# Kernel tuning notes

Measured on AMD Instinct MI355X. Metric: run time of the kernel, lower is better.

Reference implementation:

```python
import jax, jax.numpy as jnp
import numpy as np

N, E, IN_DIM, HID, OUT = 50000, 600000, 128, 256, 128

def setup_inputs() -> dict:
    key = jax.random.key(0)
    k1, k2, k3, k4, k5, k6, k7 = jax.random.split(key, 7)
    h = jax.random.normal(k1, (N, IN_DIM), dtype=jnp.float32)
    src = jax.random.randint(k2, (E,), 0, N)
    dst = jax.random.randint(k3, (E,), 0, N)
    s1 = 1.0 / np.sqrt(2 * IN_DIM)
    s2 = 1.0 / np.sqrt(HID)
    W1 = jax.random.uniform(k4, (2 * IN_DIM, HID), minval=-s1, maxval=s1, dtype=jnp.float32)
    b1 = jax.random.uniform(k5, (HID,), minval=-s1, maxval=s1, dtype=jnp.float32)
    W2 = jax.random.uniform(k6, (HID, OUT), minval=-s2, maxval=s2, dtype=jnp.float32)
    b2 = jax.random.uniform(k7, (OUT,), minval=-s2, maxval=s2, dtype=jnp.float32)
    return {"h": h, "src": src, "dst": dst, "W1": W1, "b1": b1, "W2": W2, "b2": b2}

def reference(h, src, dst, W1, b1, W2, b2):
    n = h.shape[0]
    # copy_u + mean: gather src features, segment-sum at dst, divide by in-degree
    msg_sum = jax.ops.segment_sum(h[src], dst, num_segments=n)          # [N, D]
    deg = jax.ops.segment_sum(jnp.ones((src.shape[0],), h.dtype), dst, num_segments=n)
    h_neigh = msg_sum / jnp.maximum(deg, 1.0)[:, None]                  # zero-deg nodes -> 0
    h_total = jnp.concatenate([h, h_neigh], axis=1)                     # [N, 2D]
    out = (h_total @ W1 + b1) @ W2 + b2                                 # 2-layer MLP (no inner activation)
    return jax.nn.relu(out)
```

## Files before the change

kernel.cpp:

```cpp
#include <hip/hip_runtime.h>

#define N_NODES 50000
#define E_EDGES 600000
#define IN_DIM  128
#define HID     256
#define OUT_DIM 128
#define CAP     64
#define ZROW    N_NODES

#define RANGE_N 6250
#define CHUNK_E 2048
#define NB_FILL 2344
#define NB_HCVT 3125
#define NB_WCVT 384
#define NB_PREP (NB_FILL + NB_HCVT + NB_WCVT + 1)
#define NB_MLP  782

typedef __bf16 bf16x8 __attribute__((ext_vector_type(8)));
typedef float  f32x16 __attribute__((ext_vector_type(16)));
typedef unsigned short ushort8 __attribute__((ext_vector_type(8)));

__device__ __forceinline__ unsigned short f2bf(float f) {
    union { float f; unsigned int i; } v; v.f = f;
    unsigned int b = v.i;
    b += 0x7fffu + ((b >> 16) & 1u);
    return (unsigned short)(b >> 16);
}
__device__ __forceinline__ void acc2(unsigned u, float& a0, float& a1) {
    union { unsigned i; float f; } lo, hi;
    lo.i = u << 16; hi.i = u & 0xffff0000u;
    a0 += lo.f; a1 += hi.f;
}

__global__ void __launch_bounds__(256)
sage_prep(const int* __restrict__ src, const int* __restrict__ dst,
          int* __restrict__ counts, char* __restrict__ outb,
          const float* __restrict__ h, unsigned short* __restrict__ ht,
          const float* __restrict__ W1, const float* __restrict__ W2,
          unsigned short* __restrict__ w1sw, unsigned short* __restrict__ w2sw) {
    int b = blockIdx.x;
    if (b < NB_FILL) {
        int r = b & 7;
        int chunk = b >> 3;
        int e0 = chunk * CHUNK_E + threadIdx.x * 8;
        if (e0 < E_EDGES) {
            int lo = r * RANGE_N, hi = lo + RANGE_N;
            const int4 d0 = *(const int4*)(dst + e0);
            const int4 d1 = *(const int4*)(dst + e0 + 4);
            int dd[8] = {d0.x, d0.y, d0.z, d0.w, d1.x, d1.y, d1.z, d1.w};
            #pragma unroll
            for (int k = 0; k < 8; ++k) {
                int d = dd[k];
                if (d >= lo && d < hi) {
                    int s = src[e0 + k];
                    int sl = atomicAdd(counts + d, 1);
                    if (sl < CAP) *((int*)(outb + (size_t)d * 512 + 256) + sl) = s;
                }
            }
        }
    } else if (b < NB_FILL + NB_HCVT) {
        int idx = (b - NB_FILL) * 256 + threadIdx.x;
        int n = idx >> 4, g = idx & 15;
        const float4 v0 = *(const float4*)(h + (size_t)n * IN_DIM + g * 8);
        const float4 v1 = *(const float4*)(h + (size_t)n * IN_DIM + g * 8 + 4);
        ushort8 o;
        o[0] = f2bf(v0.x); o[1] = f2bf(v0.y); o[2] = f2bf(v0.z); o[3] = f2bf(v0.w);
        o[4] = f2bf(v1.x); o[5] = f2bf(v1.y); o[6] = f2bf(v1.z); o[7] = f2bf(v1.w);
        *(ushort8*)(ht + (size_t)n * 128 + g * 8) = o;
    } else if (b < NB_FILL + NB_HCVT + NB_WCVT) {
        int i1 = (b - NB_FILL - NB_HCVT) * 256 + threadIdx.x;
        if (i1 < 65536) {
            int j = i1 & 7, n = (i1 >> 3) & 255, g = (i1 >> 11) & 1, ks = (i1 >> 12) & 3, c = i1 >> 14;
            int k = c * 64 + ks * 16 + g * 8 + j;
            w1sw[i1] = f2bf(W1[(size_t)k * HID + n]);
        } else {
            int i2 = i1 - 65536;
            int j = i2 & 7, n = (i2 >> 3) & 127, g = (i2 >> 10) & 1, ks = (i2 >> 11) & 7, c = (i2 >> 14) & 1;
            int k = c * 128 + ks * 16 + g * 8 + j;
            w2sw[i2] = f2bf(W2[(size_t)k * OUT_DIM + n]);
        }
    } else {
        if (threadIdx.x < 64)
            *(unsigned*)(ht + (size_t)ZROW * 128 + threadIdx.x * 2) = 0u;
    }
}

__global__ void __launch_bounds__(256, 4)
sage_fused(const int* __restrict__ counts,
           const unsigned short* __restrict__ ht,
           const unsigned short* __restrict__ w1sw,
           const unsigned short* __restrict__ w2sw,
           const float* __restrict__ b1,
           const float* __restrict__ b2,
           float* out) {
    __shared__ unsigned short hid_s[64][264];

    const int t = threadIdx.x;
    const int nw = t >> 6;
    const int lane = t & 63;
    const int lr = lane & 31;
    const int lg = lane >> 5;
    const int base = blockIdx.x * 64;

    {
        #pragma unroll 1
        for (int g = 0; g < 4; ++g) {
            const int m0 = nw * 16 + g * 4;
            float a0[4], a1[4];
            int deg[4], ent[4];
            const int* bk[4];
            int4 q[4];
            int em = 0;
            #pragma unroll
            for (int j = 0; j < 4; ++j) {
                a0[j] = 0.f; a1[j] = 0.f;
                int node = min(base + m0 + j, N_NODES - 1);
                deg[j] = __builtin_amdgcn_readfirstlane(counts[node]);
                ent[j] = min(deg[j], CAP);
                em = max(em, ent[j]);
                bk[j] = (const int*)((const char*)out + (size_t)node * 512 + 256);
                q[j] = *(const int4*)(bk[j]);
                unsigned self = *(const unsigned*)(ht + (size_t)node * 128 + lane * 2);
                *(unsigned*)(&hid_s[m0 + j][128 + lane * 2]) = self;
            }
            #pragma unroll 1
            for (int p = 0; p < em; p += 4) {
                int4 nx[4];
                #pragma unroll
                for (int j = 0; j < 4; ++j)
                    nx[j] = *(const int4*)(bk[j] + min(p + 4, CAP - 4));
                unsigned uu[16];
                #pragma unroll
                for (int k = 0; k < 4; ++k) {
                    #pragma unroll
                    for (int j = 0; j < 4; ++j) {
                        int idx = (k == 0) ? q[j].x : (k == 1) ? q[j].y
                                : (k == 2) ? q[j].z : q[j].w;
                        idx = __builtin_amdgcn_readfirstlane(idx);
                        idx = (p + k < ent[j]) ? idx : ZROW;
                        uu[k * 4 + j] = *(const unsigned*)(ht + (size_t)idx * 128 + lane * 2);
                    }
                }
                #pragma unroll
                for (int k = 0; k < 4; ++k) {
                    #pragma unroll
                    for (int j = 0; j < 4; ++j)
                        acc2(uu[k * 4 + j], a0[j], a1[j]);
                }
                #pragma unroll
                for (int j = 0; j < 4; ++j) q[j] = nx[j];
            }
            #pragma unroll
            for (int j = 0; j < 4; ++j) {
                float inv = 1.0f / (float)max(deg[j], 1);
                unsigned o = (unsigned)f2bf(a0[j] * inv) | ((unsigned)f2bf(a1[j] * inv) << 16);
                *(unsigned*)(&hid_s[m0 + j][lane * 2]) = o;
            }
        }
    }

    __syncthreads();

    f32x16 c1[2][2];
    #pragma unroll
    for (int e2 = 0; e2 < 16; ++e2) {
        c1[0][0][e2] = 0.f; c1[0][1][e2] = 0.f; c1[1][0][e2] = 0.f; c1[1][1][e2] = 0.f;
    }

    #pragma unroll
    for (int c = 0; c < 4; ++c) {
        bf16x8 a0[4], a1[4];
        #pragma unroll
        for (int ks = 0; ks < 4; ++ks) {
            int koff = (c < 2) ? (128 + c * 64 + ks * 16 + lg * 8)
                               : ((c - 2) * 64 + ks * 16 + lg * 8);
            a0[ks] = *(const bf16x8*)(&hid_s[lr][koff]);
            a1[ks] = *(const bf16x8*)(&hid_s[32 + lr][koff]);
        }
        #pragma unroll
        for (int ks = 0; ks < 4; ++ks) {
            #pragma unroll
            for (int nt = 0; nt < 2; ++nt) {
                int n = nw * 64 + nt * 32 + lr;
                bf16x8 b = *(const bf16x8*)(w1sw + c * 16384 + (((ks * 2 + lg) * 256) + n) * 8);
                c1[0][nt] = __builtin_amdgcn_mfma_f32_32x32x16_bf16(a0[ks], b, c1[0][nt], 0, 0, 0);
                c1[1][nt] = __builtin_amdgcn_mfma_f32_32x32x16_bf16(a1[ks], b, c1[1][nt], 0, 0, 0);
            }
        }
    }

    __syncthreads();

    #pragma unroll
    for (int nt = 0; nt < 2; ++nt) {
        int col = nw * 64 + nt * 32 + lr;
        float bias = b1[col];
        #pragma unroll
        for (int s = 0; s < 2; ++s) {
            #pragma unroll
            for (int reg = 0; reg < 16; ++reg) {
                int m = s * 32 + (reg & 3) + 8 * (reg >> 2) + 4 * lg;
                hid_s[m][col] = f2bf(c1[s][nt][reg] + bias);
            }
        }
    }
    __syncthreads();

    f32x16 c2[2];
    #pragma unroll
    for (int e2 = 0; e2 < 16; ++e2) { c2[0][e2] = 0.f; c2[1][e2] = 0.f; }

    #pragma unroll
    for (int c = 0; c < 2; ++c) {
        #pragma unroll
        for (int ks = 0; ks < 8; ++ks) {
            bf16x8 b = *(const bf16x8*)(w2sw + c * 16384 + ((ks * 2 + lg) * 128 + nw * 32 + lr) * 8);
            int koff = c * 128 + ks * 16 + lg * 8;
            bf16x8 ah0 = *(const bf16x8*)(&hid_s[lr][koff]);
            bf16x8 ah1 = *(const bf16x8*)(&hid_s[32 + lr][koff]);
            c2[0] = __builtin_amdgcn_mfma_f32_32x32x16_bf16(ah0, b, c2[0], 0, 0, 0);
            c2[1] = __builtin_amdgcn_mfma_f32_32x32x16_bf16(ah1, b, c2[1], 0, 0, 0);
        }
    }

    {
        int col = nw * 32 + lr;
        float bias = b2[col];
        #pragma unroll
        for (int s = 0; s < 2; ++s) {
            #pragma unroll
            for (int reg = 0; reg < 16; ++reg) {
                int m = s * 32 + (reg & 3) + 8 * (reg >> 2) + 4 * lg;
                int n = base + m;
                if (n < N_NODES)
                    out[(size_t)n * OUT_DIM + col] = fmaxf(c2[s][reg] + bias, 0.0f);
            }
        }
    }
}

extern "C" void kernel_launch(void* const* d_in, const int* in_sizes, int n_in,
                              void* d_out, int out_size, void* d_ws, size_t ws_size,
                              hipStream_t stream) {
    const float* h   = (const float*)d_in[0];
    const int*   src = (const int*)d_in[1];
    const int*   dst = (const int*)d_in[2];
    const float* W1  = (const float*)d_in[3];
    const float* b1  = (const float*)d_in[4];
    const float* W2  = (const float*)d_in[5];
    const float* b2  = (const float*)d_in[6];
    float* out = (float*)d_out;

    int* counts = (int*)d_ws;
    unsigned short* w1sw = (unsigned short*)(counts + N_NODES);
    unsigned short* w2sw = w1sw + 65536;
    unsigned short* ht   = w2sw + 32768;

    hipMemsetAsync(counts, 0, N_NODES * sizeof(int), stream);

    sage_prep<<<NB_PREP, 256, 0, stream>>>(
        src, dst, counts, (char*)d_out, h, ht, W1, W2, w1sw, w2sw);

    sage_fused<<<NB_MLP, 256, 0, stream>>>(counts, ht, w1sw, w2sw, b1, b2, out);
}
```

Measured before the change: 169.6 us.

## Split neighbor gather into feature-sliced kernel and co-locate bf16 features with buckets

Moves neighbor aggregation out of the fused MLP kernel into a separate gather kernel. It runs in four passes over 32-feature slices, so each pass's gathered rows fit in cache better. It gives more parallelism, with 8 nodes per wave and 4 edges processed concurrently per lane group, reduced by shuffles. The bf16 copy of h now lives in the first 256 bytes of each node's 512-byte row in the output buffer, next to its edge bucket, and the zero row is removed. The MLP kernel then reads self and mean features straight from global memory. The cost is an extra launch plus a round trip of the means array through memory.

```diff
diff --git a/kernel.cpp b/kernel.cpp
--- a/kernel.cpp
+++ b/kernel.cpp
@@ -6,14 +6,16 @@
 #define HID     256
 #define OUT_DIM 128
 #define CAP     64
-#define ZROW    N_NODES
 
 #define RANGE_N 6250
 #define CHUNK_E 2048
 #define NB_FILL 2344
 #define NB_HCVT 3125
 #define NB_WCVT 384
-#define NB_PREP (NB_FILL + NB_HCVT + NB_WCVT + 1)
+#define NB_PREP (NB_FILL + NB_HCVT + NB_WCVT)
+#define NB_GB   1563
+#define NPASS   4
+#define NB_GATHER (NPASS * NB_GB)
 #define NB_MLP  782
 
 typedef __bf16 bf16x8 __attribute__((ext_vector_type(8)));
@@ -32,10 +34,11 @@
     a0 += lo.f; a1 += hi.f;
 }
 
+
 __global__ void __launch_bounds__(256)
 sage_prep(const int* __restrict__ src, const int* __restrict__ dst,
           int* __restrict__ counts, char* __restrict__ outb,
-          const float* __restrict__ h, unsigned short* __restrict__ ht,
+          const float* __restrict__ h,
           const float* __restrict__ W1, const float* __restrict__ W2,
           unsigned short* __restrict__ w1sw, unsigned short* __restrict__ w2sw) {
     int b = blockIdx.x;
@@ -66,8 +69,8 @@
         ushort8 o;
         o[0] = f2bf(v0.x); o[1] = f2bf(v0.y); o[2] = f2bf(v0.z); o[3] = f2bf(v0.w);
         o[4] = f2bf(v1.x); o[5] = f2bf(v1.y); o[6] = f2bf(v1.z); o[7] = f2bf(v1.w);
-        *(ushort8*)(ht + (size_t)n * 128 + g * 8) = o;
-    } else if (b < NB_FILL + NB_HCVT + NB_WCVT) {
+        *(ushort8*)(outb + (size_t)n * 512 + g * 16) = o;
+    } else {
         int i1 = (b - NB_FILL - NB_HCVT) * 256 + threadIdx.x;
         if (i1 < 65536) {
             int j = i1 & 7, n = (i1 >> 3) & 255, g = (i1 >> 11) & 1, ks = (i1 >> 12) & 3, c = i1 >> 14;
@@ -79,20 +82,90 @@
             int k = c * 128 + ks * 16 + g * 8 + j;
             w2sw[i2] = f2bf(W2[(size_t)k * OUT_DIM + n]);
         }
-    } else {
-        if (threadIdx.x < 64)
-            *(unsigned*)(ht + (size_t)ZROW * 128 + threadIdx.x * 2) = 0u;
+    }
+}
+
+__global__ void __launch_bounds__(256, 8)
+sage_gather(const int* __restrict__ counts,
+            const char* __restrict__ outb,
+            unsigned short* __restrict__ means) {
+    int b = blockIdx.x;
+    int pass = b / NB_GB;
+    int nb   = b - pass * NB_GB;
+    const int t = threadIdx.x;
+    const int nw = t >> 6;
+    const int lane = t & 63;
+    const int rg = lane >> 4;
+    const int sl = lane & 15;
+    const int base = nb * 32 + nw * 8;
+    const int soff = pass * 64 + sl * 4;
+
+    float a0[8], a1[8];
+    int dg[8], ent[8], node[8];
+    const char* bkb[8];
+    int em = 0;
+    #pragma unroll
+    for (int j = 0; j < 8; ++j) {
+        node[j] = min(base + j, N_NODES - 1);
+        dg[j] = __builtin_amdgcn_readfirstlane(counts[node[j]]);
+        ent[j] = min(dg[j], CAP);
+        em = max(em, ent[j]);
+        bkb[j] = outb + (size_t)node[j] * 512 + 256;
+        a0[j] = 0.f; a1[j] = 0.f;
+    }
+
+    int idxc[8];
+    #pragma unroll
+    for (int j = 0; j < 8; ++j)
+        idxc[j] = *(const int*)(bkb[j] + rg * 4);
+
+    #pragma unroll 1
+    for (int e = 0; e < em; e += 4) {
+        int ns = min(e + 4, CAP - 4);
+        int idxn[8];
+        #pragma unroll
+        for (int j = 0; j < 8; ++j)
+            idxn[j] = *(const int*)(bkb[j] + (ns + rg) * 4);
+        int rgp = e + rg;
+        unsigned uu[8];
+        #pragma unroll
+        for (int j = 0; j < 8; ++j) {
+            int id = (rgp < ent[j]) ? idxc[j] : 0;
+            uu[j] = *(const unsigned*)(outb + (size_t)id * 512 + soff);
+        }
+        #pragma unroll
+        for (int j = 0; j < 8; ++j) {
+            unsigned v = (rgp < ent[j]) ? uu[j] : 0u;
+            acc2(v, a0[j], a1[j]);
+        }
+        #pragma unroll
+        for (int j = 0; j < 8; ++j) idxc[j] = idxn[j];
+    }
+
+    #pragma unroll
+    for (int j = 0; j < 8; ++j) {
+        a0[j] += __shfl_xor(a0[j], 16); a0[j] += __shfl_xor(a0[j], 32);
+        a1[j] += __shfl_xor(a1[j], 16); a1[j] += __shfl_xor(a1[j], 32);
+    }
+    if (rg == 0) {
+        #pragma unroll
+        for (int j = 0; j < 8; ++j) {
+            float inv = 1.0f / (float)max(dg[j], 1);
+            unsigned o = (unsigned)f2bf(a0[j] * inv) | ((unsigned)f2bf(a1[j] * inv) << 16);
+            __builtin_nontemporal_store(o,
+                (unsigned*)(means + (size_t)node[j] * 128 + pass * 32 + sl * 2));
+        }
     }
 }
 
 __global__ void __launch_bounds__(256, 4)
-sage_fused(const int* __restrict__ counts,
-           const unsigned short* __restrict__ ht,
-           const unsigned short* __restrict__ w1sw,
-           const unsigned short* __restrict__ w2sw,
-           const float* __restrict__ b1,
-           const float* __restrict__ b2,
-           float* out) {
+sage_mlp(const char* __restrict__ outb,
+         const unsigned short* __restrict__ means,
+         const unsigned short* __restrict__ w1sw,
+         const unsigned short* __restrict__ w2sw,
+         const float* __restrict__ b1,
+         const float* __restrict__ b2,
+         float* out) {
     __shared__ unsigned short hid_s[64][264];
 
     const int t = threadIdx.x;
@@ -101,65 +174,8 @@
     const int lr = lane & 31;
     const int lg = lane >> 5;
     const int base = blockIdx.x * 64;
-
-    {
-        #pragma unroll 1
-        for (int g = 0; g < 4; ++g) {
-            const int m0 = nw * 16 + g * 4;
-            float a0[4], a1[4];
-            int deg[4], ent[4];
-            const int* bk[4];
-            int4 q[4];
-            int em = 0;
-            #pragma unroll
-            for (int j = 0; j < 4; ++j) {
-                a0[j] = 0.f; a1[j] = 0.f;
-                int node = min(base + m0 + j, N_NODES - 1);
-                deg[j] = __builtin_amdgcn_readfirstlane(counts[node]);
-                ent[j] = min(deg[j], CAP);
-                em = max(em, ent[j]);
-                bk[j] = (const int*)((const char*)out + (size_t)node * 512 + 256);
-                q[j] = *(const int4*)(bk[j]);
-                unsigned self = *(const unsigned*)(ht + (size_t)node * 128 + lane * 2);
-                *(unsigned*)(&hid_s[m0 + j][128 + lane * 2]) = self;
-            }
-            #pragma unroll 1
-            for (int p = 0; p < em; p += 4) {
-                int4 nx[4];
-                #pragma unroll
-                for (int j = 0; j < 4; ++j)
-                    nx[j] = *(const int4*)(bk[j] + min(p + 4, CAP - 4));
-                unsigned uu[16];
-                #pragma unroll
-                for (int k = 0; k < 4; ++k) {
-                    #pragma unroll
-                    for (int j = 0; j < 4; ++j) {
-                        int idx = (k == 0) ? q[j].x : (k == 1) ? q[j].y
-                                : (k == 2) ? q[j].z : q[j].w;
-                        idx = __builtin_amdgcn_readfirstlane(idx);
-                        idx = (p + k < ent[j]) ? idx : ZROW;
-                        uu[k * 4 + j] = *(const unsigned*)(ht + (size_t)idx * 128 + lane * 2);
-                    }
-                }
-                #pragma unroll
-                for (int k = 0; k < 4; ++k) {
-                    #pragma unroll
-                    for (int j = 0; j < 4; ++j)
-                        acc2(uu[k * 4 + j], a0[j], a1[j]);
-                }
-                #pragma unroll
-                for (int j = 0; j < 4; ++j) q[j] = nx[j];
-            }
-            #pragma unroll
-            for (int j = 0; j < 4; ++j) {
-                float inv = 1.0f / (float)max(deg[j], 1);
-                unsigned o = (unsigned)f2bf(a0[j] * inv) | ((unsigned)f2bf(a1[j] * inv) << 16);
-                *(unsigned*)(&hid_s[m0 + j][lane * 2]) = o;
-            }
-        }
-    }
-
-    __syncthreads();
+    const int row0 = min(base + lr,      N_NODES - 1);
+    const int row1 = min(base + 32 + lr, N_NODES - 1);
 
     f32x16 c1[2][2];
     #pragma unroll
@@ -172,24 +188,27 @@
         bf16x8 a0[4], a1[4];
         #pragma unroll
         for (int ks = 0; ks < 4; ++ks) {
-            int koff = (c < 2) ? (128 + c * 64 + ks * 16 + lg * 8)
-                               : ((c - 2) * 64 + ks * 16 + lg * 8);
-            a0[ks] = *(const bf16x8*)(&hid_s[lr][koff]);
-            a1[ks] = *(const bf16x8*)(&hid_s[32 + lr][koff]);
+            if (c < 2) {
+                int kb = (c * 4 + ks) * 32 + lg * 16;
+                a0[ks] = *(const bf16x8*)(outb + (size_t)row0 * 512 + kb);
+                a1[ks] = *(const bf16x8*)(outb + (size_t)row1 * 512 + kb);
+            } else {
+                int ko = (c - 2) * 64 + ks * 16 + lg * 8;
+                a0[ks] = *(const bf16x8*)(means + (size_t)row0 * 128 + ko);
+                a1[ks] = *(const bf16x8*)(means + (size_t)row1 * 128 + ko);
+            }
         }
         #pragma unroll
         for (int ks = 0; ks < 4; ++ks) {
             #pragma unroll
             for (int nt = 0; nt < 2; ++nt) {
                 int n = nw * 64 + nt * 32 + lr;
-                bf16x8 b = *(const bf16x8*)(w1sw + c * 16384 + (((ks * 2 + lg) * 256) + n) * 8);
-                c1[0][nt] = __builtin_amdgcn_mfma_f32_32x32x16_bf16(a0[ks], b, c1[0][nt], 0, 0, 0);
-                c1[1][nt] = __builtin_amdgcn_mfma_f32_32x32x16_bf16(a1[ks], b, c1[1][nt], 0, 0, 0);
-            }
-        }
-    }
-
-    __syncthreads();
+                bf16x8 bfr = *(const bf16x8*)(w1sw + c * 16384 + (((ks * 2 + lg) * 256) + n) * 8);
+                c1[0][nt] = __builtin_amdgcn_mfma_f32_32x32x16_bf16(a0[ks], bfr, c1[0][nt], 0, 0, 0);
+                c1[1][nt] = __builtin_amdgcn_mfma_f32_32x32x16_bf16(a1[ks], bfr, c1[1][nt], 0, 0, 0);
+            }
+        }
+    }
 
     #pragma unroll
     for (int nt = 0; nt < 2; ++nt) {
@@ -214,12 +233,12 @@
     for (int c = 0; c < 2; ++c) {
         #pragma unroll
         for (int ks = 0; ks < 8; ++ks) {
-            bf16x8 b = *(const bf16x8*)(w2sw + c * 16384 + ((ks * 2 + lg) * 128 + nw * 32 + lr) * 8);
+            bf16x8 bfr = *(const bf16x8*)(w2sw + c * 16384 + ((ks * 2 + lg) * 128 + nw * 32 + lr) * 8);
             int koff = c * 128 + ks * 16 + lg * 8;
             bf16x8 ah0 = *(const bf16x8*)(&hid_s[lr][koff]);
             bf16x8 ah1 = *(const bf16x8*)(&hid_s[32 + lr][koff]);
-            c2[0] = __builtin_amdgcn_mfma_f32_32x32x16_bf16(ah0, b, c2[0], 0, 0, 0);
-            c2[1] = __builtin_amdgcn_mfma_f32_32x32x16_bf16(ah1, b, c2[1], 0, 0, 0);
+            c2[0] = __builtin_amdgcn_mfma_f32_32x32x16_bf16(ah0, bfr, c2[0], 0, 0, 0);
+            c2[1] = __builtin_amdgcn_mfma_f32_32x32x16_bf16(ah1, bfr, c2[1], 0, 0, 0);
         }
     }
 
@@ -252,14 +271,17 @@
     float* out = (float*)d_out;
 
     int* counts = (int*)d_ws;
-    unsigned short* w1sw = (unsigned short*)(counts + N_NODES);
-    unsigned short* w2sw = w1sw + 65536;
-    unsigned short* ht   = w2sw + 32768;
+    unsigned short* w1sw  = (unsigned short*)(counts + N_NODES);
+    unsigned short* w2sw  = w1sw + 65536;
+    unsigned short* means = w2sw + 32768;
 
     hipMemsetAsync(counts, 0, N_NODES * sizeof(int), stream);
 
     sage_prep<<<NB_PREP, 256, 0, stream>>>(
-        src, dst, counts, (char*)d_out, h, ht, W1, W2, w1sw, w2sw);
-
-    sage_fused<<<NB_MLP, 256, 0, stream>>>(counts, ht, w1sw, w2sw, b1, b2, out);
-}
+        src, dst, counts, (char*)d_out, h, W1, W2, w1sw, w2sw);
+
+    sage_gather<<<NB_GATHER, 256, 0, stream>>>(counts, (const char*)d_out, means);
+
+    sage_mlp<<<NB_MLP, 256, 0, stream>>>(
+        (const char*)d_out, means, w1sw, w2sw, b1, b2, out);
+}
```

After: 215.9 us. 27.3% more time.
